# Performance work log

Measured on AMD Instinct MI355X. Metric: run time of the kernel, lower is better.

## Reference

```python
import jax, jax.numpy as jnp
import numpy as np

B, T, D, U = 32, 2000, 1024, 1024
THR = 1.0  # cif_threshold


def setup_inputs() -> dict:
    key = jax.random.key(0)
    ks = jax.random.split(key, 4)
    x = jax.random.normal(ks[0], (B, T, D), jnp.float32)
    mask = jnp.zeros((B, T), dtype=bool)  # False = valid frame (no padding)
    tlen = jax.random.randint(ks[1], (B,), 100, 250)
    dense_w = jax.random.normal(ks[2], (D, U), jnp.float32) / np.sqrt(D).astype(np.float32)
    dense_b = jnp.zeros((U,), jnp.float32)
    weight_w = jax.random.normal(ks[3], (U, 1), jnp.float32) / np.sqrt(U).astype(np.float32)
    weight_b = jnp.zeros((1,), jnp.float32)
    return dict(encoder_raw_out=x, encoder_padding_mask=mask, target_lengths=tlen,
                dense_w=dense_w, dense_b=dense_b, weight_w=weight_w, weight_b=weight_b)


def _cif(x, mask, tlen, dense_w, dense_b, weight_w, weight_b):
    not_pad = (~mask).astype(x.dtype)  # [B,T], 1 = valid
    # 'dense' weight production: relu(Linear) -> Linear -> sigmoid
    h = jax.nn.relu(jnp.einsum('btd,du->btu', x, dense_w) + dense_b)
    w = jax.nn.sigmoid(jnp.einsum('btu,u->bt', h, weight_w[:, 0]) + weight_b[0])
    w = w * not_pad
    org_w = w
    # training-mode scaling so sum(weights) == target_lengths
    w = w * (tlen.astype(x.dtype) / w.sum(-1))[:, None]
    pad_start = not_pad.sum(-1)  # [B] index of first padded frame

    def step(carry, inp):
        acc_w, acc_s = carry  # [B], [B,D]
        w_t, x_t, t = inp  # [B], [B,D], scalar
        fired = acc_w + w_t >= THR  # [B]
        rem = 1.0 - acc_w
        new_w = jnp.where(fired, w_t - rem, w_t + acc_w)
        new_s = jnp.where(fired[:, None], (w_t - rem)[:, None] * x_t,
                          acc_s + w_t[:, None] * x_t)
        f_s = jnp.where(fired[:, None], acc_s + rem[:, None] * x_t, 0.0)
        f_s = jnp.where((t > pad_start)[:, None], 0.0, f_s)  # zero beyond padding start
        return (new_w, new_s), f_s

    init = (jnp.zeros((B,), x.dtype), jnp.zeros((B, D), x.dtype))
    ts = jnp.arange(T, dtype=x.dtype)
    _, fired = jax.lax.scan(step, init, (w.T, x.transpose(1, 0, 2), ts))
    fired = fired.transpose(1, 0, 2)  # [B,T,D]

    # pack fired states left-aligned (padded to T, an upper bound on fired count)
    marks = jnp.abs(fired).sum(-1) != 0.0  # [B,T]
    pos = jnp.cumsum(marks.astype(jnp.int32), axis=1) - 1
    tgt = jnp.where(marks, pos, T)  # unfired rows (all-zero) dumped into slot T
    b_idx = jnp.arange(B)[:, None]
    packed = jnp.zeros((B, T + 1, D), x.dtype).at[b_idx, tgt].add(fired)
    cif_out = packed[:, :T]
    cif_out_padding_mask = (jnp.abs(cif_out).sum(-1) != 0.0).astype(jnp.int32)
    quantity_out = org_w.sum(-1)  # training mode
    return cif_out, quantity_out, cif_out_padding_mask


def reference(encoder_raw_out, encoder_padding_mask, target_lengths,
              dense_w, dense_b, weight_w, weight_b):
    return _cif(encoder_raw_out, encoder_padding_mask, target_lengths,
                dense_w, dense_b, weight_w, weight_b)
```

## Files before the change

### kernel.cpp

```cpp
#include <hip/hip_runtime.h>
#include <cmath>

#define B_ 32
#define T_ 2000
#define D_ 1024
#define U_ 1024
#define M_ (B_*T_)
#define KCAP 256

typedef float  f32x4  __attribute__((ext_vector_type(4)));
typedef short  bf16x8 __attribute__((ext_vector_type(8)));
typedef unsigned short us4 __attribute__((ext_vector_type(4)));
typedef unsigned short us8 __attribute__((ext_vector_type(8)));
typedef __attribute__((address_space(1))) const unsigned int g_u32;
typedef __attribute__((address_space(3))) unsigned int       l_u32;

#define ZSLAB   ((T_ - KCAP) * (D_/4))
#define ZSTART  (KCAP * (D_/4))
#define BSLAB   (T_ * (D_/4))
#define ZTOTAL  ((long)B_ * ZSLAB)

__device__ __forceinline__ unsigned short bf16_rne(float f) {
    const unsigned u = __float_as_uint(f);
    return (unsigned short)((u + 0x7fffu + ((u >> 16) & 1u)) >> 16);
}

__global__ __launch_bounds__(256) void wt_conv(const float* __restrict__ W,
                                               unsigned short* __restrict__ WhT,
                                               unsigned short* __restrict__ WlT)
{
    __shared__ float tl[32][33];
    const int tx = threadIdx.x & 31, ty = threadIdx.x >> 5;
    const int n0 = blockIdx.x * 32, k0 = blockIdx.y * 32;
#pragma unroll
    for (int i = 0; i < 4; ++i)
        tl[ty + i*8][tx] = W[(size_t)(k0 + ty + i*8)*1024 + n0 + tx];
    __syncthreads();
#pragma unroll
    for (int i = 0; i < 4; ++i) {
        const float f = tl[tx][ty + i*8];
        const unsigned short h = bf16_rne(f);
        const float hif = __uint_as_float((unsigned)h << 16);
        WhT[(size_t)(n0 + ty + i*8)*1024 + k0 + tx] = h;
        WlT[(size_t)(n0 + ty + i*8)*1024 + k0 + tx] =
            (unsigned short)(__float_as_uint(f - hif) >> 16);
    }
}

__global__ __launch_bounds__(512) void xsplit(const float* __restrict__ x,
                                              unsigned short* __restrict__ Xh,
                                              float* __restrict__ out)
{
    const size_t n4 = (size_t)M_ * 1024 / 4;
    for (size_t i = (size_t)blockIdx.x * 512 + threadIdx.x; i < n4;
         i += (size_t)gridDim.x * 512) {
        const float4 v = ((const float4*)x)[i];
        us4 h;
        h[0] = bf16_rne(v.x); h[1] = bf16_rne(v.y);
        h[2] = bf16_rne(v.z); h[3] = bf16_rne(v.w);
        ((us4*)Xh)[i] = h;
    }
    float4* out4 = (float4*)out;
    const float4 zz = {0.f,0.f,0.f,0.f};
    for (long i = (long)blockIdx.x*512 + threadIdx.x; i < ZTOTAL;
         i += (long)gridDim.x*512) {
        const int b = (int)(i / ZSLAB);
        const int o = (int)(i - (long)b*ZSLAB);
        out4[(size_t)b*BSLAB + ZSTART + o] = zz;
    }
}

__global__ __launch_bounds__(512) void zfill(float* __restrict__ out)
{
    float4* out4 = (float4*)out;
    const float4 zz = {0.f,0.f,0.f,0.f};
    for (long i = (long)blockIdx.x*512 + threadIdx.x; i < ZTOTAL;
         i += (long)gridDim.x*512) {
        const int b = (int)(i / ZSLAB);
        const int o = (int)(i - (long)b*ZSLAB);
        out4[(size_t)b*BSLAB + ZSTART + o] = zz;
    }
}

__global__ __launch_bounds__(512, 1) void cif_gemm_1p(
    const unsigned short* __restrict__ Xh,
    const unsigned short* __restrict__ WhT,
    const float* __restrict__ db,
    const float* __restrict__ wvv,
    float* __restrict__ y)
{
    __shared__ unsigned short lds[2][2][256*64];
    const int tid  = threadIdx.x;
    const int lane = tid & 63;
    const int wid  = tid >> 6;
    const int wr   = wid >> 2;
    const int wc   = wid & 3;
    const int m0   = blockIdx.x * 256;
    const int li   = lane & 15, q = lane >> 4;

    const int st_r = lane >> 3;
    const int st_c = (lane & 7) ^ st_r;

    float pp[8][4];
#pragma unroll
    for (int i = 0; i < 8; ++i)
#pragma unroll
        for (int j = 0; j < 4; ++j) pp[i][j] = 0.f;

    f32x4 acc[8][4];

    auto STAGE = [&](int bf, int nb, int kt) {
        const int kbase = kt*64 + st_c*8;
#pragma unroll
        for (int j = 0; j < 4; ++j) {
            const int rg  = wid*4 + j;
            const int row = rg*8 + st_r;
            __builtin_amdgcn_global_load_lds(
                (g_u32*)(Xh + (size_t)(m0 + row)*1024 + kbase),
                (l_u32*)&lds[bf][0][rg*512], 16, 0, 0);
        }
#pragma unroll
        for (int j = 0; j < 4; ++j) {
            const int rg  = wid*4 + j;
            const int row = rg*8 + st_r;
            __builtin_amdgcn_global_load_lds(
                (g_u32*)(WhT + (size_t)(nb*256 + row)*1024 + kbase),
                (l_u32*)&lds[bf][1][rg*512], 16, 0, 0);
        }
    };

    STAGE(0, 0, 0);
    asm volatile("s_waitcnt vmcnt(0)" ::: "memory");
    __syncthreads();

    for (int it = 0; it < 64; ++it) {
        const int bf = it & 1;
        const int nb = it >> 4, kt = it & 15;
        if (kt == 0) {
#pragma unroll
            for (int i = 0; i < 8; ++i)
#pragma unroll
                for (int j = 0; j < 4; ++j) acc[i][j] = (f32x4){0.f,0.f,0.f,0.f};
        }
        if (it + 1 < 64) {
            STAGE(bf^1, (it+1) >> 4, (it+1) & 15);
            asm volatile("s_waitcnt vmcnt(8)" ::: "memory");
        } else {
            asm volatile("s_waitcnt vmcnt(0)" ::: "memory");
        }
        __builtin_amdgcn_sched_barrier(0);
        __builtin_amdgcn_s_barrier();
        __builtin_amdgcn_sched_barrier(0);

#pragma unroll
        for (int kb = 0; kb < 2; ++kb) {
            const int ch = kb*4 + q;
            bf16x8 bh[4];
#pragma unroll
            for (int nt = 0; nt < 4; ++nt) {
                const int n = wc*64 + nt*16 + li;
                bh[nt] = *(const bf16x8*)&lds[bf][1][n*64 + ((ch ^ (n&7))<<3)];
            }
#pragma unroll
            for (int mh = 0; mh < 2; ++mh) {
                bf16x8 ah[4];
#pragma unroll
                for (int m4 = 0; m4 < 4; ++m4) {
                    const int m = wr*128 + (mh*4 + m4)*16 + li;
                    ah[m4] = *(const bf16x8*)&lds[bf][0][m*64 + ((ch ^ (m&7))<<3)];
                }
#pragma unroll
                for (int m4 = 0; m4 < 4; ++m4)
#pragma unroll
                    for (int nt = 0; nt < 4; ++nt)
                        acc[mh*4+m4][nt] = __builtin_amdgcn_mfma_f32_16x16x32_bf16(
                            ah[m4], bh[nt], acc[mh*4+m4][nt], 0, 0, 0);
            }
        }
        if (kt == 15) {
#pragma unroll
            for (int nt = 0; nt < 4; ++nt) {
                const int c = nb*256 + wc*64 + nt*16 + li;
                const float dbc = db[c], wvc = wvv[c];
#pragma unroll
                for (int mt = 0; mt < 8; ++mt)
#pragma unroll
                    for (int r = 0; r < 4; ++r) {
                        float h = acc[mt][nt][r] + dbc;
                        h = fmaxf(h, 0.f);
                        pp[mt][r] = fmaf(h, wvc, pp[mt][r]);
                    }
            }
        }
        __builtin_amdgcn_sched_barrier(0);
        __builtin_amdgcn_s_barrier();
        __builtin_amdgcn_sched_barrier(0);
    }

#pragma unroll
    for (int s = 1; s < 16; s <<= 1)
#pragma unroll
        for (int mt = 0; mt < 8; ++mt)
#pragma unroll
            for (int r = 0; r < 4; ++r)
                pp[mt][r] += __shfl_xor(pp[mt][r], s, 16);
    float* red = (float*)&lds[0][0][0];
    if (li == 0) {
#pragma unroll
        for (int mt = 0; mt < 8; ++mt)
#pragma unroll
            for (int r = 0; r < 4; ++r)
                red[wc*256 + wr*128 + mt*16 + q*4 + r] = pp[mt][r];
    }
    __syncthreads();
    if (tid < 256)
        y[m0 + tid] = (red[tid] + red[256 + tid]) + (red[512 + tid] + red[768 + tid]);
}

__global__ __launch_bounds__(256, 2) void cif_gemm_fb(
    const float* __restrict__ x,
    const unsigned short* __restrict__ WhT,
    const unsigned short* __restrict__ WlT,
    const float* __restrict__ db,
    const float* __restrict__ wvv,
    float* __restrict__ y)
{
    __shared__ unsigned short Ah[128*64];
    __shared__ unsigned short Al[128*64];
    __shared__ unsigned short Bh[128*64];
    __shared__ unsigned short Bl[128*64];
    const int tid  = threadIdx.x;
    const int lane = tid & 63;
    const int wid  = tid >> 6;
    const int wr   = wid >> 1, wc = wid & 1;
    const int m0   = blockIdx.x * 128;
    const int li   = lane & 15, q = lane >> 4;

    float pp[4][4];
#pragma unroll
    for (int i = 0; i < 4; ++i)
#pragma unroll
        for (int j = 0; j < 4; ++j) pp[i][j] = 0.f;

    const int a_row = tid >> 4;
    const int a_c4  = tid & 15;
    const int b_row = tid >> 3;
    const int b_ch  = tid & 7;

    for (int nb = 0; nb < 8; ++nb) {
        f32x4 acc[4][4];
#pragma unroll
        for (int i = 0; i < 4; ++i)
#pragma unroll
            for (int j = 0; j < 4; ++j) acc[i][j] = (f32x4){0.f,0.f,0.f,0.f};

        for (int k0 = 0; k0 < 1024; k0 += 64) {
#pragma unroll
            for (int r = 0; r < 8; ++r) {
                const int m = r*16 + a_row;
                const float4 v = *(const float4*)(x + (size_t)(m0+m)*1024 + k0 + a_c4*4);
                const unsigned u0 = __float_as_uint(v.x);
                const unsigned u1 = __float_as_uint(v.y);
                const unsigned u2 = __float_as_uint(v.z);
                const unsigned u3 = __float_as_uint(v.w);
                us4 h4, l4;
                h4[0]=(unsigned short)(u0>>16); h4[1]=(unsigned short)(u1>>16);
                h4[2]=(unsigned short)(u2>>16); h4[3]=(unsigned short)(u3>>16);
                l4[0]=(unsigned short)(__float_as_uint(v.x - __uint_as_float(u0 & 0xFFFF0000u))>>16);
                l4[1]=(unsigned short)(__float_as_uint(v.y - __uint_as_float(u1 & 0xFFFF0000u))>>16);
                l4[2]=(unsigned short)(__float_as_uint(v.z - __uint_as_float(u2 & 0xFFFF0000u))>>16);
                l4[3]=(unsigned short)(__float_as_uint(v.w - __uint_as_float(u3 & 0xFFFF0000u))>>16);
                const int addr = m*64 + ((a_c4*4) ^ ((m & 7) << 3));
                *(us4*)&Ah[addr] = h4;
                *(us4*)&Al[addr] = l4;
            }
#pragma unroll
            for (int r = 0; r < 4; ++r) {
                const int n = r*32 + b_row;
                const size_t src = (size_t)(nb*128 + n)*1024 + k0 + b_ch*8;
                const int addr = n*64 + ((b_ch*8) ^ ((n & 7) << 3));
                *(us8*)&Bh[addr] = *(const us8*)(WhT + src);
                *(us8*)&Bl[addr] = *(const us8*)(WlT + src);
            }
            __syncthreads();
#pragma unroll
            for (int kb = 0; kb < 64; kb += 32) {
                bf16x8 ah[4], al[4], bh[4], bl[4];
                const int kk = kb + q*8;
#pragma unroll
                for (int mt = 0; mt < 4; ++mt) {
                    const int m = wr*64 + mt*16 + li;
                    const int addr = m*64 + (kk ^ ((m & 7) << 3));
                    ah[mt] = *(const bf16x8*)&Ah[addr];
                    al[mt] = *(const bf16x8*)&Al[addr];
                }
#pragma unroll
                for (int nt = 0; nt < 4; ++nt) {
                    const int n = wc*64 + nt*16 + li;
                    const int addr = n*64 + (kk ^ ((n & 7) << 3));
                    bh[nt] = *(const bf16x8*)&Bh[addr];
                    bl[nt] = *(const bf16x8*)&Bl[addr];
                }
#pragma unroll
                for (int mt = 0; mt < 4; ++mt)
#pragma unroll
                    for (int nt = 0; nt < 4; ++nt) {
                        acc[mt][nt] = __builtin_amdgcn_mfma_f32_16x16x32_bf16(ah[mt], bh[nt], acc[mt][nt], 0, 0, 0);
                        acc[mt][nt] = __builtin_amdgcn_mfma_f32_16x16x32_bf16(ah[mt], bl[nt], acc[mt][nt], 0, 0, 0);
                        acc[mt][nt] = __builtin_amdgcn_mfma_f32_16x16x32_bf16(al[mt], bh[nt], acc[mt][nt], 0, 0, 0);
                    }
            }
            __syncthreads();
        }
#pragma unroll
        for (int nt = 0; nt < 4; ++nt) {
            const int c = nb*128 + wc*64 + nt*16 + li;
            const float dbc = db[c], wvc = wvv[c];
#pragma unroll
            for (int mt = 0; mt < 4; ++mt)
#pragma unroll
                for (int r = 0; r < 4; ++r) {
                    float h = acc[mt][nt][r] + dbc;
                    h = fmaxf(h, 0.f);
                    pp[mt][r] = fmaf(h, wvc, pp[mt][r]);
                }
        }
    }
#pragma unroll
    for (int s = 1; s < 16; s <<= 1)
#pragma unroll
        for (int mt = 0; mt < 4; ++mt)
#pragma unroll
            for (int r = 0; r < 4; ++r)
                pp[mt][r] += __shfl_xor(pp[mt][r], s, 16);
    __syncthreads();
    float* red = (float*)Ah;
    if (li == 0) {
#pragma unroll
        for (int mt = 0; mt < 4; ++mt)
#pragma unroll
            for (int r = 0; r < 4; ++r)
                red[wc*128 + wr*64 + mt*16 + q*4 + r] = pp[mt][r];
    }
    __syncthreads();
    if (tid < 128)
        y[m0 + tid] = red[tid] + red[128 + tid];
}

__global__ __launch_bounds__(256) void cif_wns(const float* __restrict__ y,
                                               const unsigned char* __restrict__ mask,
                                               const int* __restrict__ tlen,
                                               const float* __restrict__ wb,
                                               float* __restrict__ wn,
                                               float* __restrict__ qty,
                                               int* __restrict__ fire_t,
                                               float* __restrict__ carry,
                                               int* __restrict__ nf,
                                               float* __restrict__ mout)
{
    const int b = blockIdx.x, tid = threadIdx.x;
    __shared__ float  swn[T_];
    __shared__ double sred[256];
    __shared__ int    ired[256];
    const double wbias = (double)wb[0];
    double lsum = 0.0; int lpad = 0;
    for (int t = tid; t < T_; t += 256) {
        const double z = (double)y[b*T_ + t] + wbias;
        double s = 1.0 / (1.0 + exp(-z));
        const unsigned char mk = mask[b*T_ + t];
        if (mk) s = 0.0; else ++lpad;
        swn[t] = (float)s;
        lsum += s;
    }
    for (int t = KCAP + tid; t < T_; t += 256) mout[b*T_ + t] = 0.f;
    sred[tid] = lsum; ired[tid] = lpad;
    __syncthreads();
    for (int st = 128; st > 0; st >>= 1) {
        if (tid < st) { sred[tid] += sred[tid+st]; ired[tid] += ired[tid+st]; }
        __syncthreads();
    }
    if (tid == 0) qty[b] = (float)sred[0];
    const double scale = (double)tlen[b] / sred[0];
    for (int t = tid; t < T_; t += 256) {
        const float w = (float)((double)swn[t] * scale);
        swn[t] = w;
        wn[b*T_ + t] = w;
    }
    __syncthreads();
    if (tid == 0) {
        const int pc = ired[0];
        float acc = 0.f; int k = 0;
        for (int t = 0; t < T_; ++t) {
            const float w = swn[t];
            const float s = acc + w;
            if (s >= 1.0f) {
                const float rem = 1.0f - acc;
                const float cw  = w - rem;
                if (t <= pc && k < KCAP) {
                    fire_t[b*KCAP + k] = t;
                    carry [b*KCAP + k] = cw;
                    wn[b*T_ + t] = rem;
                    ++k;
                }
                acc = cw;
            } else {
                acc = s;
            }
        }
        nf[b] = k;
    }
}

__global__ __launch_bounds__(256) void cif_scatter(const float* __restrict__ x,
                                                   const float* __restrict__ wn,
                                                   const int* __restrict__ fire_t,
                                                   const float* __restrict__ carry,
                                                   const int* __restrict__ nf,
                                                   float* __restrict__ out,
                                                   float* __restrict__ mout)
{
    const int k = blockIdx.x, b = blockIdx.y;
    const int nfb = nf[b];
    const int d = threadIdx.x * 4;
    if (threadIdx.x == 0)
        mout[b*T_ + k] = (k < nfb) ? 1.0f : 0.0f;
    float ax = 0.f, ay = 0.f, az = 0.f, aw = 0.f;
    if (k < nfb) {
        const int tk = fire_t[b*KCAP + k];
        const float* xb = x + (size_t)b * T_ * 1024;
        int ts = 0;
        if (k > 0) {
            const int   tp = fire_t[b*KCAP + k - 1];
            const float c  = carry [b*KCAP + k - 1];
            const float4 xv = *(const float4*)(xb + (size_t)tp*1024 + d);
            ax = c*xv.x; ay = c*xv.y; az = c*xv.z; aw = c*xv.w;
            ts = tp + 1;
        }
        for (int t = ts; t <= tk; ++t) {
            const float c = wn[b*T_ + t];
            const float4 xv = *(const float4*)(xb + (size_t)t*1024 + d);
            ax = fmaf(c, xv.x, ax); ay = fmaf(c, xv.y, ay);
            az = fmaf(c, xv.z, az); aw = fmaf(c, xv.w, aw);
        }
    }
    float4 r; r.x = ax; r.y = ay; r.z = az; r.w = aw;
    *(float4*)(out + ((size_t)b*T_ + k)*1024 + d) = r;
}

extern "C" void kernel_launch(void* const* d_in, const int* in_sizes, int n_in,
                              void* d_out, int out_size, void* d_ws, size_t ws_size,
                              hipStream_t stream)
{
    const float*         x    = (const float*)d_in[0];
    const unsigned char* mask = (const unsigned char*)d_in[1];
    const int*           tlen = (const int*)d_in[2];
    const float*         dW   = (const float*)d_in[3];
    const float*         db   = (const float*)d_in[4];
    const float*         wv   = (const float*)d_in[5];
    const float*         wb   = (const float*)d_in[6];

    float* out  = (float*)d_out;
    float* qty  = out + (size_t)B_*T_*D_;
    float* mout = qty + B_;

    float* ws     = (float*)d_ws;
    float* y      = ws;
    float* wn     = ws + M_;
    float* carry  = ws + 2*M_;
    int*   fire_t = (int*)(ws + 2*M_ + B_*KCAP);
    int*   nf     = (int*)(ws + 2*M_ + 2*B_*KCAP);
    size_t off = 2*(size_t)M_ + 2*B_*KCAP + 64;
    off = (off + 63) & ~(size_t)63;
    unsigned short* WhT = (unsigned short*)(ws + off);
    unsigned short* WlT = WhT + (size_t)U_*D_;
    unsigned short* Xh  = WlT + (size_t)U_*D_;
    const size_t need = off*sizeof(float)
                      + 2*(size_t)U_*D_*sizeof(unsigned short)
                      + (size_t)M_*D_*sizeof(unsigned short);

    wt_conv<<<dim3(32, 32), 256, 0, stream>>>(dW, WhT, WlT);
    if (ws_size >= need) {
        xsplit     <<<2048, 512, 0, stream>>>(x, Xh, out);
        cif_gemm_1p<<<M_/256, 512, 0, stream>>>(Xh, WhT, db, wv, y);
    } else {
        cif_gemm_fb<<<M_/128, 256, 0, stream>>>(x, WhT, WlT, db, wv, y);
        zfill      <<<2048, 512, 0, stream>>>(out);
    }
    cif_wns    <<<B_,             256, 0, stream>>>(y, mask, tlen, wb, wn, qty, fire_t, carry, nf, mout);
    cif_scatter<<<dim3(KCAP, B_), 256, 0, stream>>>(x, wn, fire_t, carry, nf, out, mout);
}
```

Measured before the change: 438.8 us.

## Split GEMM inner loop into barrier-separated phases and read bf16 x in scatter

The GEMM k-loop is restructured into four phases. Each phase loads A (and B on alternate phases) from LDS, then hits a workgroup barrier, then issues its MFMAs at raised wave priority, so that wave issue interleaves better. Separately, the scatter kernel now reads the bf16 copy of x (Xh) instead of fp32 x, halving the bytes it fetches. The fp32 path is kept for the fallback. This adds extra barriers per k-tile and lowers the precision of the output sums to bf16 inputs.

```diff
diff --git a/kernel.cpp b/kernel.cpp
--- a/kernel.cpp
+++ b/kernel.cpp
@@ -152,31 +152,37 @@
         __builtin_amdgcn_s_barrier();
         __builtin_amdgcn_sched_barrier(0);
 
-#pragma unroll
-        for (int kb = 0; kb < 2; ++kb) {
+        bf16x8 bh[4];
+#pragma unroll
+        for (int ph = 0; ph < 4; ++ph) {
+            const int kb = ph >> 1, mh = ph & 1;
             const int ch = kb*4 + q;
-            bf16x8 bh[4];
-#pragma unroll
-            for (int nt = 0; nt < 4; ++nt) {
-                const int n = wc*64 + nt*16 + li;
-                bh[nt] = *(const bf16x8*)&lds[bf][1][n*64 + ((ch ^ (n&7))<<3)];
-            }
-#pragma unroll
-            for (int mh = 0; mh < 2; ++mh) {
-                bf16x8 ah[4];
-#pragma unroll
-                for (int m4 = 0; m4 < 4; ++m4) {
-                    const int m = wr*128 + (mh*4 + m4)*16 + li;
-                    ah[m4] = *(const bf16x8*)&lds[bf][0][m*64 + ((ch ^ (m&7))<<3)];
+            if (mh == 0) {
+#pragma unroll
+                for (int nt = 0; nt < 4; ++nt) {
+                    const int n = wc*64 + nt*16 + li;
+                    bh[nt] = *(const bf16x8*)&lds[bf][1][n*64 + ((ch ^ (n&7))<<3)];
                 }
-#pragma unroll
-                for (int m4 = 0; m4 < 4; ++m4)
-#pragma unroll
-                    for (int nt = 0; nt < 4; ++nt)
-                        acc[mh*4+m4][nt] = __builtin_amdgcn_mfma_f32_16x16x32_bf16(
-                            ah[m4], bh[nt], acc[mh*4+m4][nt], 0, 0, 0);
-            }
-        }
+            }
+            bf16x8 ah[4];
+#pragma unroll
+            for (int m4 = 0; m4 < 4; ++m4) {
+                const int m = wr*128 + (mh*4 + m4)*16 + li;
+                ah[m4] = *(const bf16x8*)&lds[bf][0][m*64 + ((ch ^ (m&7))<<3)];
+            }
+            __builtin_amdgcn_sched_barrier(0);
+            __builtin_amdgcn_s_barrier();
+            __builtin_amdgcn_sched_barrier(0);
+            __builtin_amdgcn_s_setprio(1);
+#pragma unroll
+            for (int m4 = 0; m4 < 4; ++m4)
+#pragma unroll
+                for (int nt = 0; nt < 4; ++nt)
+                    acc[mh*4+m4][nt] = __builtin_amdgcn_mfma_f32_16x16x32_bf16(
+                        ah[m4], bh[nt], acc[mh*4+m4][nt], 0, 0, 0);
+            __builtin_amdgcn_s_setprio(0);
+        }
+
         if (kt == 15) {
 #pragma unroll
             for (int nt = 0; nt < 4; ++nt) {
@@ -412,6 +418,8 @@
 }
 
 __global__ __launch_bounds__(256) void cif_scatter(const float* __restrict__ x,
+                                                   const unsigned short* __restrict__ Xh,
+                                                   const int use_xh,
                                                    const float* __restrict__ wn,
                                                    const int* __restrict__ fire_t,
                                                    const float* __restrict__ carry,
@@ -427,20 +435,42 @@
     float ax = 0.f, ay = 0.f, az = 0.f, aw = 0.f;
     if (k < nfb) {
         const int tk = fire_t[b*KCAP + k];
-        const float* xb = x + (size_t)b * T_ * 1024;
         int ts = 0;
+        float c0 = 0.f; int t0 = -1;
         if (k > 0) {
-            const int   tp = fire_t[b*KCAP + k - 1];
-            const float c  = carry [b*KCAP + k - 1];
-            const float4 xv = *(const float4*)(xb + (size_t)tp*1024 + d);
-            ax = c*xv.x; ay = c*xv.y; az = c*xv.z; aw = c*xv.w;
-            ts = tp + 1;
-        }
-        for (int t = ts; t <= tk; ++t) {
-            const float c = wn[b*T_ + t];
-            const float4 xv = *(const float4*)(xb + (size_t)t*1024 + d);
-            ax = fmaf(c, xv.x, ax); ay = fmaf(c, xv.y, ay);
-            az = fmaf(c, xv.z, az); aw = fmaf(c, xv.w, aw);
+            t0 = fire_t[b*KCAP + k - 1];
+            c0 = carry [b*KCAP + k - 1];
+            ts = t0 + 1;
+        }
+        if (use_xh) {
+            const unsigned short* xb = Xh + (size_t)b * T_ * 1024;
+            if (t0 >= 0) {
+                const us4 v = *(const us4*)(xb + (size_t)t0*1024 + d);
+                ax = c0*__uint_as_float((unsigned)v[0]<<16);
+                ay = c0*__uint_as_float((unsigned)v[1]<<16);
+                az = c0*__uint_as_float((unsigned)v[2]<<16);
+                aw = c0*__uint_as_float((unsigned)v[3]<<16);
+            }
+            for (int t = ts; t <= tk; ++t) {
+                const float c = wn[b*T_ + t];
+                const us4 v = *(const us4*)(xb + (size_t)t*1024 + d);
+                ax = fmaf(c, __uint_as_float((unsigned)v[0]<<16), ax);
+                ay = fmaf(c, __uint_as_float((unsigned)v[1]<<16), ay);
+                az = fmaf(c, __uint_as_float((unsigned)v[2]<<16), az);
+                aw = fmaf(c, __uint_as_float((unsigned)v[3]<<16), aw);
+            }
+        } else {
+            const float* xb = x + (size_t)b * T_ * 1024;
+            if (t0 >= 0) {
+                const float4 xv = *(const float4*)(xb + (size_t)t0*1024 + d);
+                ax = c0*xv.x; ay = c0*xv.y; az = c0*xv.z; aw = c0*xv.w;
+            }
+            for (int t = ts; t <= tk; ++t) {
+                const float c = wn[b*T_ + t];
+                const float4 xv = *(const float4*)(xb + (size_t)t*1024 + d);
+                ax = fmaf(c, xv.x, ax); ay = fmaf(c, xv.y, ay);
+                az = fmaf(c, xv.z, az); aw = fmaf(c, xv.w, aw);
+            }
         }
     }
     float4 r; r.x = ax; r.y = ay; r.z = az; r.w = aw;
@@ -482,10 +512,12 @@
     if (ws_size >= need) {
         xsplit     <<<2048, 512, 0, stream>>>(x, Xh, out);
         cif_gemm_1p<<<M_/256, 512, 0, stream>>>(Xh, WhT, db, wv, y);
+        cif_wns    <<<B_,             256, 0, stream>>>(y, mask, tlen, wb, wn, qty, fire_t, carry, nf, mout);
+        cif_scatter<<<dim3(KCAP, B_), 256, 0, stream>>>(x, Xh, 1, wn, fire_t, carry, nf, out, mout);
     } else {
         cif_gemm_fb<<<M_/128, 256, 0, stream>>>(x, WhT, WlT, db, wv, y);
         zfill      <<<2048, 512, 0, stream>>>(out);
-    }
-    cif_wns    <<<B_,             256, 0, stream>>>(y, mask, tlen, wb, wn, qty, fire_t, carry, nf, mout);
-    cif_scatter<<<dim3(KCAP, B_), 256, 0, stream>>>(x, wn, fire_t, carry, nf, out, mout);
-}
+        cif_wns    <<<B_,             256, 0, stream>>>(y, mask, tlen, wb, wn, qty, fire_t, carry, nf, mout);
+        cif_scatter<<<dim3(KCAP, B_), 256, 0, stream>>>(x, Xh, 0, wn, fire_t, carry, nf, out, mout);
+    }
+}
```

Result: faster. 405.4 us, median of 2 (-7.6%).
